# Optimization experiments

Measured on AMD Instinct MI355X. Metric: run time of the kernel, lower is better.

Reference implementation:

```python
import jax, jax.numpy as jnp
import numpy as np
import math

D_MODEL = 768
NUM_HEADS = 12


def setup_inputs() -> dict:
    key = jax.random.key(0)
    ks = jax.random.split(key, 5)
    B, S, D = 2, 2048, D_MODEL
    scale = 1.0 / math.sqrt(D)
    x = jax.random.normal(ks[0], (B, S, D), dtype=jnp.float32)
    Wq = jax.random.normal(ks[1], (D, D), dtype=jnp.float32) * scale
    Wk = jax.random.normal(ks[2], (D, D), dtype=jnp.float32) * scale
    Wv = jax.random.normal(ks[3], (D, D), dtype=jnp.float32) * scale
    Wo = jax.random.normal(ks[4], (D, D), dtype=jnp.float32) * scale
    return {"x": x, "Wq": Wq, "Wk": Wk, "Wv": Wv, "Wo": Wo}


def _mhsa(x, Wq, Wk, Wv, Wo):
    B, S, D = x.shape
    H = NUM_HEADS
    hd = D // H
    # Linear(in, out) with weight [out, in]: y = x @ W^T
    q = x @ Wq.T
    k = x @ Wk.T
    v = x @ Wv.T
    # [B, S, H, hd] -> [B, H, S, hd]
    q = q.reshape(B, S, H, hd).transpose(0, 2, 1, 3)
    k = k.reshape(B, S, H, hd).transpose(0, 2, 1, 3)
    v = v.reshape(B, S, H, hd).transpose(0, 2, 1, 3)
    scores = jnp.einsum("bhqd,bhkd->bhqk", q, k) / jnp.sqrt(jnp.float32(hd))
    causal = jnp.tril(jnp.ones((S, S), dtype=bool))  # True where allowed
    scores = jnp.where(causal, scores, -jnp.inf)
    probs = jax.nn.softmax(scores, axis=-1)
    o = jnp.einsum("bhqk,bhkd->bhqd", probs, v)
    o = o.transpose(0, 2, 1, 3).reshape(B, S, D)
    return o @ Wo.T


def reference(x, Wq, Wk, Wv, Wo):
    return _mhsa(x, Wq, Wk, Wv, Wo)
```

## Files before the change

### kernel.cpp

```cpp
#include <hip/hip_runtime.h>
#include <math.h>

#define NHEAD 12
#define HD    64
#define SEQ   2048
#define BATCH 2
#define DM    768

typedef unsigned short u16;
typedef __attribute__((ext_vector_type(8))) short bf16x8;
typedef __attribute__((ext_vector_type(8))) unsigned short u16x8;
typedef __attribute__((ext_vector_type(4))) float f32x4;

__device__ __forceinline__ u16 f2bf(float f) {
    unsigned u = __builtin_bit_cast(unsigned, f);
    return (u16)((u + 0x7fffu + ((u >> 16) & 1u)) >> 16);
}
__device__ __forceinline__ bf16x8 as_bf16x8(uint4 v) { return __builtin_bit_cast(bf16x8, v); }
__device__ __forceinline__ u16x8  as_u16x8(uint4 v)  { return __builtin_bit_cast(u16x8, v); }
__device__ __forceinline__ f32x4 mfma16(bf16x8 a, bf16x8 b, f32x4 c) {
    return __builtin_amdgcn_mfma_f32_16x16x32_bf16(a, b, c, 0, 0, 0);
}

__global__ void cvt4(const float* __restrict__ s, u16* __restrict__ d, int n4) {
    int i = blockIdx.x * blockDim.x + threadIdx.x;
    if (i < n4) {
        float4 v = ((const float4*)s)[i];
        ushort4 o;
        o.x = f2bf(v.x); o.y = f2bf(v.y); o.z = f2bf(v.z); o.w = f2bf(v.w);
        ((ushort4*)d)[i] = o;
    }
}

__global__ void cvt4w(const float* __restrict__ s0, const float* __restrict__ s1,
                      const float* __restrict__ s2, const float* __restrict__ s3,
                      u16* __restrict__ d0, u16* __restrict__ d1,
                      u16* __restrict__ d2, u16* __restrict__ d3, int n4) {
    const float* s = blockIdx.y == 0 ? s0 : blockIdx.y == 1 ? s1 : blockIdx.y == 2 ? s2 : s3;
    u16*         d = blockIdx.y == 0 ? d0 : blockIdx.y == 1 ? d1 : blockIdx.y == 2 ? d2 : d3;
    int i = blockIdx.x * blockDim.x + threadIdx.x;
    if (i < n4) {
        float4 v = ((const float4*)s)[i];
        ushort4 o;
        o.x = f2bf(v.x); o.y = f2bf(v.y); o.z = f2bf(v.z); o.w = f2bf(v.w);
        ((ushort4*)d)[i] = o;
    }
}

__global__ __launch_bounds__(256)
void qkv_mfma(const u16* __restrict__ X,
              const u16* __restrict__ Wq, const u16* __restrict__ Wk,
              const u16* __restrict__ Wv,
              u16* __restrict__ Q, u16* __restrict__ K, u16* __restrict__ V)
{
    const u16* W = blockIdx.z == 0 ? Wq : blockIdx.z == 1 ? Wk : Wv;
    u16*       Y = blockIdx.z == 0 ? Q  : blockIdx.z == 1 ? K  : V;
    const float osc = (blockIdx.z == 0) ? 0.125f : 1.0f;
    const int m0 = blockIdx.x * 128, n0 = blockIdx.y * 128;

    __shared__ __align__(16) u16 As[128 * 40];
    __shared__ __align__(16) u16 Bs[128 * 40];

    const int tid = threadIdx.x;
    const int w = tid >> 6, l = tid & 63, lg = l >> 4, lr = l & 15;
    const int wr = w >> 1, wc = w & 1;
    const int srow = tid >> 1, sh = tid & 1;

    const u16* ga = X + (size_t)(m0 + srow) * DM + sh * 16;
    const u16* gb = W + (size_t)(n0 + srow) * DM + sh * 16;
    const int sidx = srow * 40 + sh * 16;

    f32x4 acc[4][4];
    #pragma unroll
    for (int i = 0; i < 4; ++i)
        #pragma unroll
        for (int j = 0; j < 4; ++j) acc[i][j] = (f32x4){0.f, 0.f, 0.f, 0.f};

    for (int k0 = 0; k0 < DM; k0 += 32) {
        uint4 a0 = *(const uint4*)(ga + k0);
        uint4 a1 = *(const uint4*)(ga + k0 + 8);
        uint4 b0 = *(const uint4*)(gb + k0);
        uint4 b1 = *(const uint4*)(gb + k0 + 8);
        __syncthreads();
        *(uint4*)&As[sidx] = a0; *(uint4*)&As[sidx + 8] = a1;
        *(uint4*)&Bs[sidx] = b0; *(uint4*)&Bs[sidx + 8] = b1;
        __syncthreads();
        bf16x8 af[4], bfr[4];
        #pragma unroll
        for (int i = 0; i < 4; ++i) {
            af[i]  = as_bf16x8(*(const uint4*)&As[(wr * 64 + i * 16 + lr) * 40 + lg * 8]);
            bfr[i] = as_bf16x8(*(const uint4*)&Bs[(wc * 64 + i * 16 + lr) * 40 + lg * 8]);
        }
        __builtin_amdgcn_s_setprio(1);
        #pragma unroll
        for (int i = 0; i < 4; ++i)
            #pragma unroll
            for (int j = 0; j < 4; ++j)
                acc[i][j] = mfma16(af[i], bfr[j], acc[i][j]);
        __builtin_amdgcn_s_setprio(0);
    }

    #pragma unroll
    for (int i = 0; i < 4; ++i) {
        const int mb = m0 + wr * 64 + i * 16 + lg * 4;
        #pragma unroll
        for (int j = 0; j < 4; ++j) {
            const int n = n0 + wc * 64 + j * 16 + lr;
            const int h = n >> 6, dc = n & 63;
            #pragma unroll
            for (int r = 0; r < 4; ++r) {
                const int m = mb + r;
                const int b = m >> 11, s2 = m & 2047;
                Y[(((size_t)b * NHEAD + h) * SEQ + s2) * HD + dc] = f2bf(acc[i][j][r] * osc);
            }
        }
    }
}

__global__ __launch_bounds__(256)
void attn_mfma(const u16* __restrict__ Qg, const u16* __restrict__ Kg,
               const u16* __restrict__ Vg, u16* __restrict__ Og)
{
    const int q0 = (31 - blockIdx.x) * 64;
    const int bh = blockIdx.y;
    const int kend = q0 >> 6;
    const size_t base = (size_t)bh * SEQ * HD;
    const u16* Qb = Qg + base;
    const u16* Kb = Kg + base;
    const u16* Vb = Vg + base;
    u16*       Ob = Og + base;

    __shared__ __align__(16) u16 Ks[64 * 64];
    __shared__ __align__(16) u16 Vt[64 * 64];

    const int tid = threadIdx.x;
    const int w = tid >> 6, l = tid & 63, lg = l >> 4, lr = l & 15;

    const int srow = w * 16 + (l >> 2);
    const int c0   = (l & 3) * 16;

    const int qrow = q0 + w * 16 + lr;
    bf16x8 qf[2];
    #pragma unroll
    for (int kh = 0; kh < 2; ++kh)
        qf[kh] = as_bf16x8(*(const uint4*)(Qb + (size_t)qrow * HD + kh * 32 + lg * 8));

    float ms = -INFINITY, lsum = 0.f;
    f32x4 ov[4];
    #pragma unroll
    for (int dj = 0; dj < 4; ++dj) ov[dj] = (f32x4){0.f, 0.f, 0.f, 0.f};

    for (int kt = 0; kt <= kend; ++kt) {
        const int k0 = kt * 64;

        const u16* kp = Kb + (size_t)(k0 + srow) * HD + c0;
        const u16* vp = Vb + (size_t)(k0 + srow) * HD + c0;
        uint4 kq0 = *(const uint4*)(kp);
        uint4 kq1 = *(const uint4*)(kp + 8);
        uint4 vq0 = *(const uint4*)(vp);
        uint4 vq1 = *(const uint4*)(vp + 8);

        __syncthreads();
        {
            const int sw = (srow & 7) << 4;
            *(uint4*)&Ks[srow * 64 + (((c0 * 2) ^ sw) >> 1)]        = kq0;
            *(uint4*)&Ks[srow * 64 + ((((c0 + 8) * 2) ^ sw) >> 1)]  = kq1;
        }
        #pragma unroll
        for (int h = 0; h < 2; ++h) {
            u16x8 vv = as_u16x8(h ? vq1 : vq0);
            #pragma unroll
            for (int e = 0; e < 8; ++e) {
                const int d  = c0 + h * 8 + e;
                const int cs = (d & 7) ^ ((d >> 3) & 7);
                Vt[d * 64 + (((srow * 2) ^ (cs << 4)) >> 1)] = vv[e];
            }
        }
        __syncthreads();

        f32x4 sc[4];
        #pragma unroll
        for (int nj = 0; nj < 4; ++nj) sc[nj] = (f32x4){0.f, 0.f, 0.f, 0.f};
        __builtin_amdgcn_s_setprio(1);
        #pragma unroll
        for (int kh = 0; kh < 2; ++kh) {
            #pragma unroll
            for (int nj = 0; nj < 4; ++nj) {
                const int s  = nj * 16 + lr;
                const int cb = kh * 64 + lg * 16;
                bf16x8 kf = as_bf16x8(*(const uint4*)&Ks[s * 64 + ((cb ^ ((s & 7) << 4)) >> 1)]);
                sc[nj] = mfma16(kf, qf[kh], sc[nj]);
            }
        }
        __builtin_amdgcn_s_setprio(0);

        if (kt == kend) {
            #pragma unroll
            for (int nj = 0; nj < 4; ++nj)
                #pragma unroll
                for (int r = 0; r < 4; ++r) {
                    const int key = k0 + nj * 16 + lg * 4 + r;
                    if (key > qrow) sc[nj][r] = -INFINITY;
                }
        }

        float pm = sc[0][0];
        #pragma unroll
        for (int nj = 0; nj < 4; ++nj)
            #pragma unroll
            for (int r = 0; r < 4; ++r) pm = fmaxf(pm, sc[nj][r]);
        pm = fmaxf(pm, __shfl_xor(pm, 16));
        pm = fmaxf(pm, __shfl_xor(pm, 32));

        if (!__all(pm <= ms + 8.f)) {
            const float mn  = fmaxf(ms, pm);
            const float fac = __expf(ms - mn);
            ms = mn;
            lsum *= fac;
            const int fi = __builtin_bit_cast(int, fac);
            #pragma unroll
            for (int r = 0; r < 4; ++r) {
                const float fr = __builtin_bit_cast(float,
                    __builtin_amdgcn_ds_bpermute((lg * 4 + r) * 4, fi));
                #pragma unroll
                for (int dj = 0; dj < 4; ++dj) ov[dj][r] *= fr;
            }
        }

        float rs = 0.f;
        #pragma unroll
        for (int nj = 0; nj < 4; ++nj)
            #pragma unroll
            for (int r = 0; r < 4; ++r) {
                const float p = __expf(sc[nj][r] - ms);
                sc[nj][r] = p;
                rs += p;
            }
        rs += __shfl_xor(rs, 16);
        rs += __shfl_xor(rs, 32);
        lsum += rs;

        unsigned pw[4][2];
        #pragma unroll
        for (int nj = 0; nj < 4; ++nj) {
            asm("v_cvt_pk_bf16_f32 %0, %1, %2" : "=v"(pw[nj][0]) : "v"(sc[nj][0]), "v"(sc[nj][1]));
            asm("v_cvt_pk_bf16_f32 %0, %1, %2" : "=v"(pw[nj][1]) : "v"(sc[nj][2]), "v"(sc[nj][3]));
        }

        __builtin_amdgcn_s_setprio(1);
        #pragma unroll
        for (int ks = 0; ks < 2; ++ks) {
            uint4 pa4;
            pa4.x = pw[2 * ks][0]; pa4.y = pw[2 * ks][1];
            pa4.z = pw[2 * ks + 1][0]; pa4.w = pw[2 * ks + 1][1];
            const bf16x8 pa = as_bf16x8(pa4);
            const int b0 = 64 * ks + 8 * lg;
            #pragma unroll
            for (int dj = 0; dj < 4; ++dj) {
                const int d  = dj * 16 + lr;
                const int cs = (d & 7) ^ ((d >> 3) & 7);
                const uint2 v0 = *(const uint2*)&Vt[d * 64 + ((b0 ^ (cs << 4)) >> 1)];
                const uint2 v1 = *(const uint2*)&Vt[d * 64 + (((b0 + 32) ^ (cs << 4)) >> 1)];
                uint4 vv; vv.x = v0.x; vv.y = v0.y; vv.z = v1.x; vv.w = v1.y;
                ov[dj] = mfma16(pa, as_bf16x8(vv), ov[dj]);
            }
        }
        __builtin_amdgcn_s_setprio(0);
    }

    const int li = __builtin_bit_cast(int, lsum);
    #pragma unroll
    for (int r = 0; r < 4; ++r) {
        const float lrow = __builtin_bit_cast(float,
            __builtin_amdgcn_ds_bpermute((lg * 4 + r) * 4, li));
        const float inv = 1.0f / lrow;
        const int row = q0 + w * 16 + lg * 4 + r;
        #pragma unroll
        for (int dj = 0; dj < 4; ++dj)
            Ob[(size_t)row * HD + dj * 16 + lr] = f2bf(ov[dj][r] * inv);
    }
}

__global__ __launch_bounds__(256)
void proj_mfma(const u16* __restrict__ O, const u16* __restrict__ Wo,
               float* __restrict__ out)
{
    const int m0 = blockIdx.x * 128, n0 = blockIdx.y * 128;

    __shared__ __align__(16) u16 As[128 * 40];
    __shared__ __align__(16) u16 Bs[128 * 40];

    const int tid = threadIdx.x;
    const int w = tid >> 6, l = tid & 63, lg = l >> 4, lr = l & 15;
    const int wr = w >> 1, wc = w & 1;
    const int srow = tid >> 1, sh = tid & 1;

    const int m = m0 + srow;
    const int b = m >> 11, s2 = m & 2047;
    const u16* gb = Wo + (size_t)(n0 + srow) * DM + sh * 16;
    const int sidx = srow * 40 + sh * 16;

    f32x4 acc[4][4];
    #pragma unroll
    for (int i = 0; i < 4; ++i)
        #pragma unroll
        for (int j = 0; j < 4; ++j) acc[i][j] = (f32x4){0.f, 0.f, 0.f, 0.f};

    for (int k0 = 0; k0 < DM; k0 += 32) {
        const int kk = k0 + sh * 16;
        const u16* ga = O + (((size_t)b * NHEAD + (kk >> 6)) * SEQ + s2) * HD + (kk & 63);
        uint4 a0 = *(const uint4*)(ga);
        uint4 a1 = *(const uint4*)(ga + 8);
        uint4 b0 = *(const uint4*)(gb + k0);
        uint4 b1 = *(const uint4*)(gb + k0 + 8);
        __syncthreads();
        *(uint4*)&As[sidx] = a0; *(uint4*)&As[sidx + 8] = a1;
        *(uint4*)&Bs[sidx] = b0; *(uint4*)&Bs[sidx + 8] = b1;
        __syncthreads();
        bf16x8 af[4], bfr[4];
        #pragma unroll
        for (int i = 0; i < 4; ++i) {
            af[i]  = as_bf16x8(*(const uint4*)&As[(wr * 64 + i * 16 + lr) * 40 + lg * 8]);
            bfr[i] = as_bf16x8(*(const uint4*)&Bs[(wc * 64 + i * 16 + lr) * 40 + lg * 8]);
        }
        __builtin_amdgcn_s_setprio(1);
        #pragma unroll
        for (int i = 0; i < 4; ++i)
            #pragma unroll
            for (int j = 0; j < 4; ++j)
                acc[i][j] = mfma16(af[i], bfr[j], acc[i][j]);
        __builtin_amdgcn_s_setprio(0);
    }

    #pragma unroll
    for (int i = 0; i < 4; ++i) {
        const int mb = m0 + wr * 64 + i * 16 + lg * 4;
        #pragma unroll
        for (int j = 0; j < 4; ++j) {
            const int n = n0 + wc * 64 + j * 16 + lr;
            #pragma unroll
            for (int r = 0; r < 4; ++r)
                out[(size_t)(mb + r) * DM + n] = acc[i][j][r];
        }
    }
}

extern "C" void kernel_launch(void* const* d_in, const int* in_sizes, int n_in,
                              void* d_out, int out_size, void* d_ws, size_t ws_size,
                              hipStream_t stream)
{
    const float* x  = (const float*)d_in[0];
    const float* Wq = (const float*)d_in[1];
    const float* Wk = (const float*)d_in[2];
    const float* Wv = (const float*)d_in[3];
    const float* Wo = (const float*)d_in[4];
    float* out = (float*)d_out;

    const size_t nx = (size_t)BATCH * SEQ * DM;
    const size_t nw = (size_t)DM * DM;
    const size_t nh = (size_t)BATCH * NHEAD * SEQ * HD;

    u16* xb  = (u16*)d_ws;
    u16* wqb = xb  + nx;
    u16* wkb = wqb + nw;
    u16* wvb = wkb + nw;
    u16* wob = wvb + nw;
    u16* Qb  = wob + nw;
    u16* Kb  = Qb  + nh;
    u16* Vb  = Kb  + nh;
    u16* Ob  = Vb  + nh;

    cvt4<<<(int)(nx / 4 / 256), 256, 0, stream>>>(x, xb, (int)(nx / 4));
    dim3 gw((unsigned)(nw / 4 / 256), 4);
    cvt4w<<<gw, 256, 0, stream>>>(Wq, Wk, Wv, Wo, wqb, wkb, wvb, wob, (int)(nw / 4));

    dim3 g1(BATCH * SEQ / 128, DM / 128, 3);
    qkv_mfma<<<g1, 256, 0, stream>>>(xb, wqb, wkb, wvb, Qb, Kb, Vb);

    dim3 g2(32, BATCH * NHEAD);
    attn_mfma<<<g2, 256, 0, stream>>>(Qb, Kb, Vb, Ob);

    dim3 g3(BATCH * SEQ / 128, DM / 128);
    proj_mfma<<<g3, 256, 0, stream>>>(Ob, wob, out);
}
```

Baseline: 209.5 us.

## Double-buffer GEMM tiles via direct global-to-LDS loads with XOR swizzle

The QKV and output-projection GEMMs now stage tiles with global_load_lds straight into LDS, skipping the round trip through registers. LDS is double-buffered so the next k-slice is fetched while MFMAs run on the current one, and the per-iteration barriers drop from two to one. Padded rows are replaced by an XOR column swizzle to avoid bank conflicts. The risks are correctness of the async LDS writes relative to the single barrier (no explicit vmcnt wait) and doubled LDS use per block.

```diff
diff --git a/kernel.cpp b/kernel.cpp
--- a/kernel.cpp
+++ b/kernel.cpp
@@ -12,6 +12,9 @@
 typedef __attribute__((ext_vector_type(8))) unsigned short u16x8;
 typedef __attribute__((ext_vector_type(4))) float f32x4;
 
+typedef const __attribute__((address_space(1))) unsigned int gu32;
+typedef __attribute__((address_space(3))) unsigned int lu32;
+
 __device__ __forceinline__ u16 f2bf(float f) {
     unsigned u = __builtin_bit_cast(unsigned, f);
     return (u16)((u + 0x7fffu + ((u >> 16) & 1u)) >> 16);
@@ -20,6 +23,9 @@
 __device__ __forceinline__ u16x8  as_u16x8(uint4 v)  { return __builtin_bit_cast(u16x8, v); }
 __device__ __forceinline__ f32x4 mfma16(bf16x8 a, bf16x8 b, f32x4 c) {
     return __builtin_amdgcn_mfma_f32_16x16x32_bf16(a, b, c, 0, 0, 0);
+}
+__device__ __forceinline__ void gl16(const u16* g, u16* l) {
+    __builtin_amdgcn_global_load_lds((gu32*)g, (lu32*)l, 16, 0, 0);
 }
 
 __global__ void cvt4(const float* __restrict__ s, u16* __restrict__ d, int n4) {
@@ -58,17 +64,14 @@
     const float osc = (blockIdx.z == 0) ? 0.125f : 1.0f;
     const int m0 = blockIdx.x * 128, n0 = blockIdx.y * 128;
 
-    __shared__ __align__(16) u16 As[128 * 40];
-    __shared__ __align__(16) u16 Bs[128 * 40];
+    __shared__ __align__(16) u16 As[2][128 * 32];
+    __shared__ __align__(16) u16 Bs[2][128 * 32];
 
     const int tid = threadIdx.x;
     const int w = tid >> 6, l = tid & 63, lg = l >> 4, lr = l & 15;
     const int wr = w >> 1, wc = w & 1;
-    const int srow = tid >> 1, sh = tid & 1;
-
-    const u16* ga = X + (size_t)(m0 + srow) * DM + sh * 16;
-    const u16* gb = W + (size_t)(n0 + srow) * DM + sh * 16;
-    const int sidx = srow * 40 + sh * 16;
+    const int Lr = l >> 2;
+    const int cg = (l & 3) ^ (Lr & 3);
 
     f32x4 acc[4][4];
     #pragma unroll
@@ -76,20 +79,28 @@
         #pragma unroll
         for (int j = 0; j < 4; ++j) acc[i][j] = (f32x4){0.f, 0.f, 0.f, 0.f};
 
-    for (int k0 = 0; k0 < DM; k0 += 32) {
-        uint4 a0 = *(const uint4*)(ga + k0);
-        uint4 a1 = *(const uint4*)(ga + k0 + 8);
-        uint4 b0 = *(const uint4*)(gb + k0);
-        uint4 b1 = *(const uint4*)(gb + k0 + 8);
-        __syncthreads();
-        *(uint4*)&As[sidx] = a0; *(uint4*)&As[sidx + 8] = a1;
-        *(uint4*)&Bs[sidx] = b0; *(uint4*)&Bs[sidx + 8] = b1;
-        __syncthreads();
+    auto STAGE = [&](int buf, int k0) {
+        #pragma unroll
+        for (int c = 0; c < 2; ++c) {
+            const int rb = w * 32 + c * 16;
+            const int r  = rb + Lr;
+            gl16(X + (size_t)(m0 + r) * DM + k0 + cg * 8, &As[buf][rb * 32]);
+            gl16(W + (size_t)(n0 + r) * DM + k0 + cg * 8, &Bs[buf][rb * 32]);
+        }
+    };
+
+    int cur = 0;
+    STAGE(0, 0);
+    __syncthreads();
+
+    const int ro = (lg ^ (lr & 3)) * 8;
+    for (int t = 0; t < 24; ++t) {
+        if (t < 23) STAGE(cur ^ 1, (t + 1) * 32);
         bf16x8 af[4], bfr[4];
         #pragma unroll
         for (int i = 0; i < 4; ++i) {
-            af[i]  = as_bf16x8(*(const uint4*)&As[(wr * 64 + i * 16 + lr) * 40 + lg * 8]);
-            bfr[i] = as_bf16x8(*(const uint4*)&Bs[(wc * 64 + i * 16 + lr) * 40 + lg * 8]);
+            af[i]  = as_bf16x8(*(const uint4*)&As[cur][(wr * 64 + i * 16 + lr) * 32 + ro]);
+            bfr[i] = as_bf16x8(*(const uint4*)&Bs[cur][(wc * 64 + i * 16 + lr) * 32 + ro]);
         }
         __builtin_amdgcn_s_setprio(1);
         #pragma unroll
@@ -98,6 +109,8 @@
             for (int j = 0; j < 4; ++j)
                 acc[i][j] = mfma16(af[i], bfr[j], acc[i][j]);
         __builtin_amdgcn_s_setprio(0);
+        __syncthreads();
+        cur ^= 1;
     }
 
     #pragma unroll
@@ -287,18 +300,14 @@
 {
     const int m0 = blockIdx.x * 128, n0 = blockIdx.y * 128;
 
-    __shared__ __align__(16) u16 As[128 * 40];
-    __shared__ __align__(16) u16 Bs[128 * 40];
+    __shared__ __align__(16) u16 As[2][128 * 32];
+    __shared__ __align__(16) u16 Bs[2][128 * 32];
 
     const int tid = threadIdx.x;
     const int w = tid >> 6, l = tid & 63, lg = l >> 4, lr = l & 15;
     const int wr = w >> 1, wc = w & 1;
-    const int srow = tid >> 1, sh = tid & 1;
-
-    const int m = m0 + srow;
-    const int b = m >> 11, s2 = m & 2047;
-    const u16* gb = Wo + (size_t)(n0 + srow) * DM + sh * 16;
-    const int sidx = srow * 40 + sh * 16;
+    const int Lr = l >> 2;
+    const int cg = (l & 3) ^ (Lr & 3);
 
     f32x4 acc[4][4];
     #pragma unroll
@@ -306,22 +315,34 @@
         #pragma unroll
         for (int j = 0; j < 4; ++j) acc[i][j] = (f32x4){0.f, 0.f, 0.f, 0.f};
 
-    for (int k0 = 0; k0 < DM; k0 += 32) {
-        const int kk = k0 + sh * 16;
-        const u16* ga = O + (((size_t)b * NHEAD + (kk >> 6)) * SEQ + s2) * HD + (kk & 63);
-        uint4 a0 = *(const uint4*)(ga);
-        uint4 a1 = *(const uint4*)(ga + 8);
-        uint4 b0 = *(const uint4*)(gb + k0);
-        uint4 b1 = *(const uint4*)(gb + k0 + 8);
-        __syncthreads();
-        *(uint4*)&As[sidx] = a0; *(uint4*)&As[sidx + 8] = a1;
-        *(uint4*)&Bs[sidx] = b0; *(uint4*)&Bs[sidx + 8] = b1;
-        __syncthreads();
+    auto STAGE = [&](int buf, int k0) {
+        #pragma unroll
+        for (int c = 0; c < 2; ++c) {
+            const int rb = w * 32 + c * 16;
+            const int r  = rb + Lr;
+            {
+                const int m = m0 + r;
+                const int b = m >> 11, s2 = m & 2047;
+                const int k = k0 + cg * 8;
+                const int h = k >> 6, dk = k & 63;
+                gl16(O + (((size_t)b * NHEAD + h) * SEQ + s2) * HD + dk, &As[buf][rb * 32]);
+            }
+            gl16(Wo + (size_t)(n0 + r) * DM + k0 + cg * 8, &Bs[buf][rb * 32]);
+        }
+    };
+
+    int cur = 0;
+    STAGE(0, 0);
+    __syncthreads();
+
+    const int ro = (lg ^ (lr & 3)) * 8;
+    for (int t = 0; t < 24; ++t) {
+        if (t < 23) STAGE(cur ^ 1, (t + 1) * 32);
         bf16x8 af[4], bfr[4];
         #pragma unroll
         for (int i = 0; i < 4; ++i) {
-            af[i]  = as_bf16x8(*(const uint4*)&As[(wr * 64 + i * 16 + lr) * 40 + lg * 8]);
-            bfr[i] = as_bf16x8(*(const uint4*)&Bs[(wc * 64 + i * 16 + lr) * 40 + lg * 8]);
+            af[i]  = as_bf16x8(*(const uint4*)&As[cur][(wr * 64 + i * 16 + lr) * 32 + ro]);
+            bfr[i] = as_bf16x8(*(const uint4*)&Bs[cur][(wc * 64 + i * 16 + lr) * 32 + ro]);
         }
         __builtin_amdgcn_s_setprio(1);
         #pragma unroll
@@ -330,6 +351,8 @@
             for (int j = 0; j < 4; ++j)
                 acc[i][j] = mfma16(af[i], bfr[j], acc[i][j]);
         __builtin_amdgcn_s_setprio(0);
+        __syncthreads();
+        cur ^= 1;
     }
 
     #pragma unroll
```

Measured after the change: 204.1 us. 1.03x faster.
